# Performance work log

Hardware: AMD Instinct MI355X
Metric: run time of the kernel (lower is better)

## Reference

```python
import jax, jax.numpy as jnp
import numpy as np

N = 17
H = 8
DIRECT = np.array([[0,1],[1,2],[2,3],[0,4],[4,5],[5,6],[0,7],[7,8],[8,9],[9,10],[8,11],[11,12],[12,13],[8,14],[14,15],[15,16]])
SYM = np.array([[1,4],[2,5],[3,6],[11,14],[12,15],[13,16]])


def _base_mask(dw, sw, cw):
    # static skeleton bias: ones + direct-connect + symmetric + self-connect weights
    m = jnp.ones((N, N), jnp.float32)
    m = m.at[DIRECT[:, 0], DIRECT[:, 1]].add(dw)
    m = m.at[SYM[:, 0], SYM[:, 1]].add(sw)
    m = m.at[SYM[:, 1], SYM[:, 0]].add(sw)
    return m + cw * jnp.eye(N, dtype=jnp.float32)


def _ln_custom(x, g, b, eps=1e-6):
    # custom LayerNorm: unbiased std (torch .std default), eps added to std
    mu = x.mean(-1, keepdims=True)
    var = ((x - mu) ** 2).sum(-1, keepdims=True) / (x.shape[-1] - 1)
    return g * (x - mu) / (jnp.sqrt(var) + eps) + b


def _ln_std(x, g, b, eps=1e-5):
    # standard nn.LayerNorm (biased var, eps inside sqrt)
    mu = x.mean(-1, keepdims=True)
    var = ((x - mu) ** 2).mean(-1, keepdims=True)
    return g * (x - mu) * jax.lax.rsqrt(var + eps) + b


def _forward(mask, x, pre_3d, c, wq, bq, wk, bk, wv, bv, wo, bo, sa_w1, sa_b1, sa_g1, sa_sb1, sa_w2, sa_b2, sa_g2, sa_sb2, jrp_w, jrp_b, direct_w, sym_w, self_w, dyn_scale, A_hat, g1_w, g1_b, g2_w, g2_b, n1_g, n1_b, n2_g, n2_b, ada1_w, ada1_b, ada2_w, ada2_b):
    B, _, D = x.shape
    dk = D // H
    inv = 1.0 / np.sqrt(dk)
    mflag = (mask == 0)[:, None]                       # [B,1,N,N]
    sil_c = jax.nn.silu(c)
    for i in range(wq.shape[0]):                       # small fixed layer count
        # --- sublayer 0: adaLN-modulated skeleton-biased self-attention ---
        sh1, sc1, gt1 = jnp.split(sil_c @ ada1_w[i] + ada1_b[i], 3, axis=2)
        xin = _ln_custom(x, n1_g[i], n1_b[i]) * (1 + sc1) + sh1
        Q = (pre_3d @ wq[i] + bq[i]).reshape(B, N, H, dk).transpose(0, 2, 1, 3)
        K = (xin @ wk[i] + bk[i]).reshape(B, N, H, dk).transpose(0, 2, 1, 3)
        V = (xin @ wv[i] + bv[i]).reshape(B, N, H, dk).transpose(0, 2, 1, 3)
        scores = jnp.einsum('bhqd,bhkd->bhqk', Q, K) * inv
        # dynamic skeleton mask from query features (pre_3d)
        jf = jax.nn.relu(_ln_std(pre_3d @ sa_w1[i] + sa_b1[i], sa_g1[i], sa_sb1[i]))
        jf = jax.nn.relu(_ln_std(jf @ sa_w2[i] + sa_b2[i], sa_g2[i], sa_sb2[i]))
        dyn = jax.nn.sigmoid(jf @ jrp_w[i] + jrp_b[i]) * dyn_scale[i]   # [B,N,N]
        skel = _base_mask(direct_w[i], sym_w[i], self_w[i])[None] + dyn
        guided = jnp.where(mflag, -1e9, scores * skel[:, None])
        p = jax.nn.softmax(guided, axis=-1)
        att = jnp.einsum('bhqk,bhkd->bhqd', p, V).transpose(0, 2, 1, 3).reshape(B, N, D)
        x = x + gt1 * (att @ wo[i] + bo[i])
        # --- sublayer 1: adaLN-modulated GraphNet (2 Laplacian gconvs) ---
        sh2, sc2, gt2 = jnp.split(sil_c @ ada2_w[i] + ada2_b[i], 3, axis=2)
        y = _ln_custom(x, n2_g[i], n2_b[i]) * (1 + sc2) + sh2
        a = A_hat[i]
        dh = (a.sum(0) + 1e-5) ** -0.5                  # column-degree^{-1/2}
        Lm = dh[:, None] * a * dh[None, :]
        y0 = jax.nn.relu(jnp.einsum('ij,bjd->bid', Lm, y) @ g1_w[i] + g1_b[i])
        y1 = jnp.einsum('ij,bjd->bid', Lm, y0) @ g2_w[i] + g2_b[i]
        x = x + gt2 * y1
    return x


def setup_inputs():
    B, D, Lyr = 4096, 256, 2
    ki = iter(jax.random.split(jax.random.key(0), 32))
    rn = lambda *s: jax.random.normal(next(ki), s, jnp.float32) * 0.02
    z = lambda *s: jnp.zeros(s, jnp.float32)
    o = lambda *s: jnp.ones(s, jnp.float32)
    return {
        'x': jax.random.normal(next(ki), (B, N, D), jnp.float32),
        'pre_3d': jax.random.normal(next(ki), (B, N, D), jnp.float32),
        'c': jax.random.normal(next(ki), (B, N, D), jnp.float32),
        'mask': jnp.ones((B, N, N), jnp.int32),
        'wq': rn(Lyr, D, D), 'bq': z(Lyr, D),
        'wk': rn(Lyr, D, D), 'bk': z(Lyr, D),
        'wv': rn(Lyr, D, D), 'bv': z(Lyr, D),
        'wo': rn(Lyr, D, D), 'bo': z(Lyr, D),
        'sa_w1': rn(Lyr, D, D // 2), 'sa_b1': z(Lyr, D // 2),
        'sa_g1': o(Lyr, D // 2), 'sa_sb1': z(Lyr, D // 2),
        'sa_w2': rn(Lyr, D // 2, D // 4), 'sa_b2': z(Lyr, D // 4),
        'sa_g2': o(Lyr, D // 4), 'sa_sb2': z(Lyr, D // 4),
        'jrp_w': rn(Lyr, D // 4, N), 'jrp_b': z(Lyr, N),
        'direct_w': jnp.full((Lyr,), 2.0, jnp.float32),
        'sym_w': jnp.full((Lyr,), 1.5, jnp.float32),
        'self_w': jnp.full((Lyr,), 3.0, jnp.float32),
        'dyn_scale': jnp.full((Lyr,), 0.5, jnp.float32),
        'A_hat': jnp.tile(jnp.eye(N, dtype=jnp.float32)[None], (Lyr, 1, 1)),
        'g1_w': rn(Lyr, D, 2 * D), 'g1_b': z(Lyr, 2 * D),
        'g2_w': rn(Lyr, 2 * D, D), 'g2_b': z(Lyr, D),
        'n1_g': o(Lyr, D), 'n1_b': z(Lyr, D),
        'n2_g': o(Lyr, D), 'n2_b': z(Lyr, D),
        'ada1_w': rn(Lyr, D, 3 * D), 'ada1_b': z(Lyr, 3 * D),
        'ada2_w': rn(Lyr, D, 3 * D), 'ada2_b': z(Lyr, 3 * D),
    }


def reference(x, pre_3d, c, mask, wq, bq, wk, bk, wv, bv, wo, bo, sa_w1, sa_b1, sa_g1, sa_sb1, sa_w2, sa_b2, sa_g2, sa_sb2, jrp_w, jrp_b, direct_w, sym_w, self_w, dyn_scale, A_hat, g1_w, g1_b, g2_w, g2_b, n1_g, n1_b, n2_g, n2_b, ada1_w, ada1_b, ada2_w, ada2_b):
    return _forward(mask, x, pre_3d, c, wq, bq, wk, bk, wv, bv, wo, bo, sa_w1, sa_b1, sa_g1, sa_sb1, sa_w2, sa_b2, sa_g2, sa_sb2, jrp_w, jrp_b, direct_w, sym_w, self_w, dyn_scale, A_hat, g1_w, g1_b, g2_w, g2_b, n1_g, n1_b, n2_g, n2_b, ada1_w, ada1_b, ada2_w, ada2_b)
```

## Files before the change

kernel.cpp:

```cpp
#include <hip/hip_runtime.h>
#include <stdint.h>


#define BATCH 4096
#define NJ 17
#define NHEAD 8

typedef __bf16 bf16x8 __attribute__((ext_vector_type(8)));
typedef float f32x4 __attribute__((ext_vector_type(4)));

__device__ __forceinline__ float bf2f(unsigned short u){
  union { unsigned int i; float f; } v; v.i = ((unsigned int)u) << 16; return v.f;
}
__device__ __forceinline__ unsigned short f2bf(float f){
  union { float f; unsigned int i; } v; v.f = f;
  unsigned int i = v.i;
  return (unsigned short)((i + 0x7fffu + ((i >> 16) & 1u)) >> 16);
}
__device__ __forceinline__ float blo(unsigned int v){ union{unsigned int i;float f;}x; x.i=v<<16; return x.f; }
__device__ __forceinline__ float bhi(unsigned int v){ union{unsigned int i;float f;}x; x.i=v&0xffff0000u; return x.f; }

__device__ __forceinline__ void gload_lds16(const void* g, void* l) {
  __builtin_amdgcn_global_load_lds(
      (const __attribute__((address_space(1))) unsigned int*)g,
      (__attribute__((address_space(3))) unsigned int*)l, 16, 0, 0);
}

__global__ __launch_bounds__(256) void prep_kernel(
    const float* __restrict__ pre, const float* __restrict__ c,
    unsigned short* __restrict__ pre_bf, unsigned short* __restrict__ silc_bf)
{
  size_t i = (size_t)(blockIdx.x*256 + threadIdx.x)*4;
  float4 p = *(const float4*)(pre + i);
  float4 cv = *(const float4*)(c + i);
  float s0 = cv.x/(1.f+__expf(-cv.x));
  float s1 = cv.y/(1.f+__expf(-cv.y));
  float s2 = cv.z/(1.f+__expf(-cv.z));
  float s3 = cv.w/(1.f+__expf(-cv.w));
  uint2 po, so;
  po.x = (unsigned)f2bf(p.x) | ((unsigned)f2bf(p.y)<<16);
  po.y = (unsigned)f2bf(p.z) | ((unsigned)f2bf(p.w)<<16);
  so.x = (unsigned)f2bf(s0) | ((unsigned)f2bf(s1)<<16);
  so.y = (unsigned)f2bf(s2) | ((unsigned)f2bf(s3)<<16);
  *(uint2*)(pre_bf + i) = po;
  *(uint2*)(silc_bf + i) = so;
}

struct TJob { const float* src; unsigned short* dst; int K; int N; };
struct TJobs { TJob j[22]; };

__global__ __launch_bounds__(256) void transpose_kernel(TJobs jobs)
{
  TJob jb = jobs.j[blockIdx.y];
  int total = jb.K * jb.N;
  int idx = blockIdx.x*256 + threadIdx.x;
  if (idx >= total) return;
  int n = idx / jb.K;
  int k = idx - n*jb.K;
  jb.dst[idx] = f2bf(jb.src[(size_t)k*jb.N + n]);
}

__global__ void lm_kernel(const float* __restrict__ A_hat, float* __restrict__ LmOut)
{
  int L = blockIdx.x;
  const float* a = A_hat + L*289;
  float* Lm = LmOut + L*289;
  __shared__ float dh[17];
  int t = threadIdx.x;
  if (t < 17) {
    float s = 0;
    for (int i = 0; i < 17; i++) s += a[i*17 + t];
    dh[t] = 1.0f/sqrtf(s + 1e-5f);
  }
  __syncthreads();
  for (int i = t; i < 289; i += 64) {
    int qq = i/17, jj = i - qq*17;
    Lm[i] = dh[qq]*a[i]*dh[jj];
  }
}

__global__ __launch_bounds__(256) void lnmod_kernel(
    const float* __restrict__ x, const unsigned short* __restrict__ shsc,
    const float* __restrict__ g, const float* __restrict__ b,
    unsigned short* __restrict__ out)
{
  int row = blockIdx.x*4 + (threadIdx.x>>6);
  int lane = threadIdx.x & 63;
  const float4 v = *(const float4*)(x + (size_t)row*256 + lane*4);
  float s = v.x+v.y+v.z+v.w;
#pragma unroll
  for (int o=32;o;o>>=1) s += __shfl_down(s,o,64);
  float mu = __shfl(s,0,64) * (1.f/256.f);
  float d0=v.x-mu,d1=v.y-mu,d2=v.z-mu,d3=v.w-mu;
  float qq = d0*d0+d1*d1+d2*d2+d3*d3;
#pragma unroll
  for (int o=32;o;o>>=1) qq += __shfl_down(qq,o,64);
  qq = __shfl(qq,0,64);
  float rstd = 1.f/(sqrtf(qq*(1.f/255.f)) + 1e-6f);
  int c = lane*4;
  const float4 gv = *(const float4*)(g + c);
  const float4 bv = *(const float4*)(b + c);
  const uint2 shp = *(const uint2*)(shsc + (size_t)row*512 + c);
  const uint2 scp = *(const uint2*)(shsc + (size_t)row*512 + 256 + c);
  float o0 = (gv.x*d0*rstd + bv.x)*(1.f+blo(scp.x)) + blo(shp.x);
  float o1 = (gv.y*d1*rstd + bv.y)*(1.f+bhi(scp.x)) + bhi(shp.x);
  float o2 = (gv.z*d2*rstd + bv.z)*(1.f+blo(scp.y)) + blo(shp.y);
  float o3 = (gv.w*d3*rstd + bv.w)*(1.f+bhi(scp.y)) + bhi(shp.y);
  uint2 ov;
  ov.x = (unsigned)f2bf(o0) | ((unsigned)f2bf(o1)<<16);
  ov.y = (unsigned)f2bf(o2) | ((unsigned)f2bf(o3)<<16);
  *(uint2*)(out + (size_t)row*256 + c) = ov;
}

template<int C>
__global__ __launch_bounds__(256) void lnstd_relu_kernel(
    unsigned short* __restrict__ io, const float* __restrict__ g, const float* __restrict__ b)
{
  constexpr int EPL = C/64;
  int row = blockIdx.x*4 + (threadIdx.x>>6);
  int lane = threadIdx.x & 63;
  unsigned short* rp = io + (size_t)row*C + lane*EPL;
  float v[EPL];
  if constexpr (EPL == 2) { unsigned int u = *(const unsigned int*)rp; v[0]=blo(u); v[1]=bhi(u); }
  else { v[0] = bf2f(rp[0]); }
  float s = 0;
#pragma unroll
  for (int e=0;e<EPL;e++) s += v[e];
#pragma unroll
  for (int o=32;o;o>>=1) s += __shfl_down(s,o,64);
  float mu = __shfl(s,0,64) * (1.f/C);
  float qq = 0;
#pragma unroll
  for (int e=0;e<EPL;e++){ float d=v[e]-mu; qq += d*d; }
#pragma unroll
  for (int o=32;o;o>>=1) qq += __shfl_down(qq,o,64);
  qq = __shfl(qq,0,64);
  float rstd = rsqrtf(qq*(1.f/C) + 1e-5f);
  unsigned short ov[EPL];
#pragma unroll
  for (int e=0;e<EPL;e++){
    int ccol = lane*EPL + e;
    float o = fmaxf(g[ccol]*(v[e]-mu)*rstd + b[ccol], 0.f);
    ov[e] = f2bf(o);
  }
  if constexpr (EPL==2){ *(unsigned int*)rp = (unsigned)ov[0] | ((unsigned)ov[1]<<16); }
  else rp[0] = ov[0];
}

__global__ __launch_bounds__(256) void skel_kernel(
    const unsigned short* __restrict__ jf2, const unsigned short* __restrict__ jrpt,
    const float* __restrict__ jrp_b,
    const float* __restrict__ dwp, const float* __restrict__ swp,
    const float* __restrict__ cwp, const float* __restrict__ dsp,
    float* __restrict__ skel)
{
  int gid = blockIdx.x*256 + threadIdx.x;
  int row = gid / 17;
  int k = gid - row*17;
  int q = row % 17;
  const uint4* a = (const uint4*)(jf2 + (size_t)row*64);
  const uint4* w = (const uint4*)(jrpt + k*64);
  float acc = jrp_b[k];
#pragma unroll
  for (int c = 0; c < 8; c++) {
    uint4 ua = a[c], uw = w[c];
    acc += blo(ua.x)*blo(uw.x) + bhi(ua.x)*bhi(uw.x)
         + blo(ua.y)*blo(uw.y) + bhi(ua.y)*bhi(uw.y)
         + blo(ua.z)*blo(uw.z) + bhi(ua.z)*bhi(uw.z)
         + blo(ua.w)*blo(uw.w) + bhi(ua.w)*bhi(uw.w);
  }
  float sig = 1.f/(1.f + __expf(-acc));
  float base = 1.f;
  const int dqa[16] = {0,1,2,0,4,5,0,7,8,9,8,11,12,8,14,15};
  const int dka[16] = {1,2,3,4,5,6,7,8,9,10,11,12,13,14,15,16};
#pragma unroll
  for (int t = 0; t < 16; t++) if (q==dqa[t] && k==dka[t]) base += dwp[0];
  const int s0a[6] = {1,2,3,11,12,13};
  const int s1a[6] = {4,5,6,14,15,16};
#pragma unroll
  for (int t = 0; t < 6; t++) if ((q==s0a[t]&&k==s1a[t])||(q==s1a[t]&&k==s0a[t])) base += swp[0];
  if (q==k) base += cwp[0];
  skel[gid] = base + sig*dsp[0];
}

__device__ __forceinline__ void load32(const unsigned short* p, float* f){
  const uint4* p4 = (const uint4*)p;
#pragma unroll
  for (int c=0;c<4;c++){
    uint4 u=p4[c];
    f[c*8+0]=blo(u.x); f[c*8+1]=bhi(u.x); f[c*8+2]=blo(u.y); f[c*8+3]=bhi(u.y);
    f[c*8+4]=blo(u.z); f[c*8+5]=bhi(u.z); f[c*8+6]=blo(u.w); f[c*8+7]=bhi(u.w);
  }
}

__global__ __launch_bounds__(256) void attn_kernel(
    const unsigned short* Q, const unsigned short* __restrict__ Kb,
    const unsigned short* __restrict__ V, const float* __restrict__ skel,
    const int* __restrict__ mask, unsigned short* att)
{
  int tid = blockIdx.x*256 + threadIdx.x;
  int b = tid / 136;
  int r = tid - b*136;
  int h = r / 17;
  int q = r - h*17;
  size_t rq = ((size_t)(b*17+q))*256 + h*32;
  float qv[32];
  load32(Q + rq, qv);
  const float* sk = skel + (size_t)(b*17+q)*17;
  const int* mk = mask + (size_t)b*289 + q*17;
  float p[17];
  float mx = -3e38f;
#pragma unroll
  for (int k = 0; k < 17; k++) {
    const uint4* kp = (const uint4*)(Kb + ((size_t)(b*17+k))*256 + h*32);
    float s = 0;
#pragma unroll
    for (int c = 0; c < 4; c++) {
      uint4 u = kp[c];
      s += qv[c*8+0]*blo(u.x) + qv[c*8+1]*bhi(u.x)
         + qv[c*8+2]*blo(u.y) + qv[c*8+3]*bhi(u.y)
         + qv[c*8+4]*blo(u.z) + qv[c*8+5]*bhi(u.z)
         + qv[c*8+6]*blo(u.w) + qv[c*8+7]*bhi(u.w);
    }
    s *= 0.17677669529663687f;
    float gvl = (mk[k]==0) ? -1e9f : s*sk[k];
    p[k] = gvl;
    mx = fmaxf(mx, gvl);
  }
  float sum = 0;
#pragma unroll
  for (int k = 0; k < 17; k++){ p[k] = __expf(p[k]-mx); sum += p[k]; }
  float inv = 1.f/sum;
  float acc[32];
#pragma unroll
  for (int d=0; d<32; d++) acc[d]=0;
#pragma unroll
  for (int k = 0; k < 17; k++) {
    float pk = p[k]*inv;
    const uint4* vp = (const uint4*)(V + ((size_t)(b*17+k))*256 + h*32);
#pragma unroll
    for (int c=0;c<4;c++){
      uint4 u=vp[c];
      acc[c*8+0] += pk*blo(u.x); acc[c*8+1] += pk*bhi(u.x);
      acc[c*8+2] += pk*blo(u.y); acc[c*8+3] += pk*bhi(u.y);
      acc[c*8+4] += pk*blo(u.z); acc[c*8+5] += pk*bhi(u.z);
      acc[c*8+6] += pk*blo(u.w); acc[c*8+7] += pk*bhi(u.w);
    }
  }
  uint4 o[4];
#pragma unroll
  for (int c=0;c<4;c++){
    o[c].x = (unsigned)f2bf(acc[c*8+0]) | ((unsigned)f2bf(acc[c*8+1])<<16);
    o[c].y = (unsigned)f2bf(acc[c*8+2]) | ((unsigned)f2bf(acc[c*8+3])<<16);
    o[c].z = (unsigned)f2bf(acc[c*8+4]) | ((unsigned)f2bf(acc[c*8+5])<<16);
    o[c].w = (unsigned)f2bf(acc[c*8+6]) | ((unsigned)f2bf(acc[c*8+7])<<16);
  }
  uint4* op = (uint4*)(att + rq);
#pragma unroll
  for (int c=0;c<4;c++) op[c] = o[c];
}

template<int D>
__global__ __launch_bounds__(256) void lmapply_kernel(
    unsigned short* __restrict__ io, const float* __restrict__ Lm)
{
  __shared__ unsigned short ys[17*D];
  __shared__ float lms[289];
  int b = blockIdx.x;
  int tid = threadIdx.x;
  unsigned short* base = io + (size_t)b*17*D;
  constexpr int CH = 17*D/8;
  for (int i = tid; i < CH; i += 256) ((uint4*)ys)[i] = ((const uint4*)base)[i];
  for (int i = tid; i < 289; i += 256) lms[i] = Lm[i];
  __syncthreads();
#pragma unroll
  for (int c0 = 0; c0 < D; c0 += 256) {
    int c = c0 + tid;
    float yv[17];
#pragma unroll
    for (int j = 0; j < 17; j++) yv[j] = bf2f(ys[j*D + c]);
#pragma unroll
    for (int qi = 0; qi < 17; qi++) {
      float a = 0;
#pragma unroll
      for (int j = 0; j < 17; j++) a += lms[qi*17+j]*yv[j];
      base[qi*D + c] = f2bf(a);
    }
  }
}

template<int TM, int TN, int EPI>
__global__ __launch_bounds__(256) void gemm_kernel(
    const unsigned short* __restrict__ A, const unsigned short* __restrict__ Bt,
    const float* __restrict__ bias, unsigned short* __restrict__ outbf,
    float* __restrict__ x_io, const unsigned short* __restrict__ gt,
    int N, int K)
{
  int lane = threadIdx.x & 63;
  int wave = threadIdx.x >> 6;
  int lm = lane & 15, quad = lane >> 4;
  int wm0 = blockIdx.x*(2*TM*16) + (wave>>1)*(TM*16);
  int wn0 = blockIdx.y*(2*TN*16) + (wave&1)*(TN*16);
  const unsigned short* pa[TM];
  const unsigned short* pb[TN];
#pragma unroll
  for (int t=0;t<TM;t++) pa[t] = A + (size_t)(wm0 + t*16 + lm)*K + quad*8;
#pragma unroll
  for (int t=0;t<TN;t++) pb[t] = Bt + (size_t)(wn0 + t*16 + lm)*K + quad*8;
  f32x4 acc[TM][TN] = {};
  for (int kc = 0; kc < K; kc += 32) {
    bf16x8 af[TM], bfv[TN];
#pragma unroll
    for (int t=0;t<TM;t++) af[t] = *(const bf16x8*)(pa[t] + kc);
#pragma unroll
    for (int t=0;t<TN;t++) bfv[t] = *(const bf16x8*)(pb[t] + kc);
#pragma unroll
    for (int i=0;i<TM;i++)
#pragma unroll
      for (int j=0;j<TN;j++)
        acc[i][j] = __builtin_amdgcn_mfma_f32_16x16x32_bf16(af[i], bfv[j], acc[i][j], 0, 0, 0);
  }
#pragma unroll
  for (int j=0;j<TN;j++) {
    int col = wn0 + j*16 + lm;
    float bv = bias[col];
#pragma unroll
    for (int i=0;i<TM;i++) {
      int r0 = wm0 + i*16 + quad*4;
#pragma unroll
      for (int e=0;e<4;e++) {
        int rr = r0 + e;
        float v = acc[i][j][e] + bv;
        if (EPI == 0) {
          outbf[(size_t)rr*N + col] = f2bf(v);
        } else if (EPI == 1) {
          outbf[(size_t)rr*N + col] = f2bf(fmaxf(v, 0.f));
        } else {
          size_t xi = (size_t)rr*N + col;
          x_io[xi] += bf2f(gt[(size_t)rr*256 + col]) * v;
        }
      }
    }
  }
}

template<int EPI>
__global__ __launch_bounds__(256) void gemm_lds_kernel(
    const unsigned short* __restrict__ A, const unsigned short* __restrict__ Bt,
    const float* __restrict__ bias, unsigned short* __restrict__ outbf,
    float* __restrict__ x_io, const unsigned short* __restrict__ gt,
    int N, int K)
{
  __shared__ unsigned short As[128*32];
  __shared__ unsigned short Bs[128*32];
  const int tid = threadIdx.x;
  const int lane = tid & 63;
  const int wave = tid >> 6;
  const int lm = lane & 15, quad = lane >> 4;
  const int m0 = blockIdx.y * 128;
  const int n0 = blockIdx.x * 128;
  const int wm = (wave >> 1) * 64;
  const int wn = (wave & 1) * 64;

  const int srow = tid >> 2;
  const int sslot = tid & 3;

  f32x4 acc[4][4] = {};

  for (int kc = 0; kc < K; kc += 32) {
    __syncthreads();
#pragma unroll
    for (int l = 0; l < 2; l++) {
      int r = l*64 + srow;
      int gs = sslot ^ (r & 3);
      gload_lds16(A + (size_t)(m0 + r)*K + kc + gs*8, As + (size_t)l*2048 + tid*8);
      gload_lds16(Bt + (size_t)(n0 + r)*K + kc + gs*8, Bs + (size_t)l*2048 + tid*8);
    }
    __syncthreads();

    bf16x8 af[4], bfv[4];
#pragma unroll
    for (int t = 0; t < 4; t++) {
      int ra = wm + t*16 + lm;
      af[t]  = *(const bf16x8*)(As + ra*32 + ((quad ^ (ra & 3)) << 3));
      int rb = wn + t*16 + lm;
      bfv[t] = *(const bf16x8*)(Bs + rb*32 + ((quad ^ (rb & 3)) << 3));
    }
#pragma unroll
    for (int i = 0; i < 4; i++)
#pragma unroll
      for (int j = 0; j < 4; j++)
        acc[i][j] = __builtin_amdgcn_mfma_f32_16x16x32_bf16(af[i], bfv[j], acc[i][j], 0, 0, 0);
  }

#pragma unroll
  for (int j = 0; j < 4; j++) {
    int col = n0 + wn + j*16 + lm;
    float bv = bias[col];
#pragma unroll
    for (int i = 0; i < 4; i++) {
      int r0 = m0 + wm + i*16 + quad*4;
#pragma unroll
      for (int e = 0; e < 4; e++) {
        int rr = r0 + e;
        float v = acc[i][j][e] + bv;
        if (EPI == 0) {
          outbf[(size_t)rr*N + col] = f2bf(v);
        } else if (EPI == 1) {
          outbf[(size_t)rr*N + col] = f2bf(fmaxf(v, 0.f));
        } else {
          size_t xi = (size_t)rr*N + col;
          x_io[xi] += bf2f(gt[(size_t)rr*256 + col]) * v;
        }
      }
    }
  }
}

extern "C" void kernel_launch(void* const* d_in, const int* in_sizes, int n_in,
                              void* d_out, int out_size, void* d_ws, size_t ws_size,
                              hipStream_t stream)
{
  const float* x_in = (const float*)d_in[0];
  const float* pre  = (const float*)d_in[1];
  const float* cc   = (const float*)d_in[2];
  const int*   mask = (const int*)d_in[3];
  const float* wq = (const float*)d_in[4];   const float* bq = (const float*)d_in[5];
  const float* wk = (const float*)d_in[6];   const float* bk = (const float*)d_in[7];
  const float* wv = (const float*)d_in[8];   const float* bv = (const float*)d_in[9];
  const float* wo = (const float*)d_in[10];  const float* bo = (const float*)d_in[11];
  const float* sa_w1 = (const float*)d_in[12]; const float* sa_b1 = (const float*)d_in[13];
  const float* sa_g1 = (const float*)d_in[14]; const float* sa_sb1 = (const float*)d_in[15];
  const float* sa_w2 = (const float*)d_in[16]; const float* sa_b2 = (const float*)d_in[17];
  const float* sa_g2 = (const float*)d_in[18]; const float* sa_sb2 = (const float*)d_in[19];
  const float* jrp_w = (const float*)d_in[20]; const float* jrp_b = (const float*)d_in[21];
  const float* dwp = (const float*)d_in[22]; const float* swp = (const float*)d_in[23];
  const float* cwp = (const float*)d_in[24]; const float* dsp = (const float*)d_in[25];
  const float* A_hat = (const float*)d_in[26];
  const float* g1w = (const float*)d_in[27]; const float* g1b = (const float*)d_in[28];
  const float* g2w = (const float*)d_in[29]; const float* g2b = (const float*)d_in[30];
  const float* n1g = (const float*)d_in[31]; const float* n1b = (const float*)d_in[32];
  const float* n2g = (const float*)d_in[33]; const float* n2b = (const float*)d_in[34];
  const float* ada1w = (const float*)d_in[35]; const float* ada1b = (const float*)d_in[36];
  const float* ada2w = (const float*)d_in[37]; const float* ada2b = (const float*)d_in[38];

  char* ws = (char*)d_ws;
  size_t off = 0;
  auto alloc = [&](size_t bytes)->char* {
    char* p = ws + off; off = (off + bytes + 255) & ~(size_t)255; return p;
  };

  TJobs jobs;
  int ji = 0;
  auto addjob = [&](const float* src, int Kd, int Nd)->unsigned short* {
    unsigned short* dst = (unsigned short*)alloc((size_t)Kd*Nd*2);
    jobs.j[ji].src = src; jobs.j[ji].dst = dst; jobs.j[ji].K = Kd; jobs.j[ji].N = Nd;
    ji++;
    return dst;
  };
  unsigned short *t_ada1[2], *t_wq[2], *t_wk[2], *t_wv[2], *t_wo[2],
                 *t_sa1[2], *t_sa2[2], *t_jrp[2], *t_g1[2], *t_g2[2], *t_ada2[2];
  for (int L = 0; L < 2; L++) {
    t_ada1[L] = addjob(ada1w + (size_t)L*256*768, 256, 768);
    t_wq[L]   = addjob(wq + (size_t)L*65536, 256, 256);
    t_wk[L]   = addjob(wk + (size_t)L*65536, 256, 256);
    t_wv[L]   = addjob(wv + (size_t)L*65536, 256, 256);
    t_wo[L]   = addjob(wo + (size_t)L*65536, 256, 256);
    t_sa1[L]  = addjob(sa_w1 + (size_t)L*256*128, 256, 128);
    t_sa2[L]  = addjob(sa_w2 + (size_t)L*128*64, 128, 64);
    t_jrp[L]  = addjob(jrp_w + (size_t)L*64*17, 64, 17);
    t_g1[L]   = addjob(g1w + (size_t)L*256*512, 256, 512);
    t_g2[L]   = addjob(g2w + (size_t)L*512*256, 512, 256);
    t_ada2[L] = addjob(ada2w + (size_t)L*256*768, 256, 768);
  }
  float* lmbuf = (float*)alloc(2*289*4);
  size_t fixed_bytes = off;

  int chunkB = BATCH;
  for (; chunkB > 256; chunkB >>= 1) {
    size_t R = (size_t)chunkB * NJ;
    if (fixed_bytes + R*3652 + 8*256 <= ws_size) break;
  }
  const size_t R = (size_t)chunkB * NJ;
  const int nchunks = BATCH / chunkB;

  unsigned short* pre_bf  = (unsigned short*)alloc(R*256*2);
  unsigned short* silc_bf = (unsigned short*)alloc(R*256*2);
  unsigned short* xinb    = (unsigned short*)alloc(R*256*2);
  unsigned short* qbuf    = (unsigned short*)alloc(R*256*2);
  unsigned short* gtbuf   = (unsigned short*)alloc(R*256*2);
  unsigned short* kvb     = (unsigned short*)alloc(R*512*2);
  float*          skelb   = (float*)alloc(R*NJ*4);

  unsigned short* jf1 = xinb;
  unsigned short* jf2 = xinb + R*128;
  unsigned short* Kbuf = kvb;
  unsigned short* Vbuf = kvb + R*256;

  float* xout = (float*)d_out;
  hipMemcpyAsync(xout, x_in, (size_t)BATCH*NJ*256*4, hipMemcpyDeviceToDevice, stream);
  transpose_kernel<<<dim3(768, 22), 256, 0, stream>>>(jobs);
  lm_kernel<<<2, 64, 0, stream>>>(A_hat, lmbuf);

  const int gX = (int)(R/128);
  const int g4 = (int)(R/4);

  for (int ch = 0; ch < nchunks; ch++) {
    const size_t r0 = (size_t)ch * R;
    const float* pre_c = pre + r0*256;
    const float* cc_c  = cc + r0*256;
    const int* mask_c  = mask + (size_t)ch*chunkB*289;
    float* x_c = xout + r0*256;

    prep_kernel<<<g4, 256, 0, stream>>>(pre_c, cc_c, pre_bf, silc_bf);

    for (int L = 0; L < 2; L++) {
      gemm_lds_kernel<0><<<dim3(4,gX),256,0,stream>>>(silc_bf, t_ada1[L], ada1b + L*768, kvb, nullptr, nullptr, 512, 256);
      gemm_lds_kernel<0><<<dim3(2,gX),256,0,stream>>>(silc_bf, t_ada1[L] + 512*256, ada1b + L*768 + 512, gtbuf, nullptr, nullptr, 256, 256);
      lnmod_kernel<<<g4,256,0,stream>>>(x_c, kvb, n1g + L*256, n1b + L*256, xinb);
      gemm_lds_kernel<0><<<dim3(2,gX),256,0,stream>>>(pre_bf, t_wq[L], bq + L*256, qbuf, nullptr, nullptr, 256, 256);
      gemm_lds_kernel<0><<<dim3(2,gX),256,0,stream>>>(xinb, t_wk[L], bk + L*256, Kbuf, nullptr, nullptr, 256, 256);
      gemm_lds_kernel<0><<<dim3(2,gX),256,0,stream>>>(xinb, t_wv[L], bv + L*256, Vbuf, nullptr, nullptr, 256, 256);
      gemm_lds_kernel<0><<<dim3(1,gX),256,0,stream>>>(pre_bf, t_sa1[L], sa_b1 + L*128, jf1, nullptr, nullptr, 128, 256);
      lnstd_relu_kernel<128><<<g4,256,0,stream>>>(jf1, sa_g1 + L*128, sa_sb1 + L*128);
      gemm_kernel<4,2,0><<<dim3(gX,1),256,0,stream>>>(jf1, t_sa2[L], sa_b2 + L*64, jf2, nullptr, nullptr, 64, 128);
      lnstd_relu_kernel<64><<<g4,256,0,stream>>>(jf2, sa_g2 + L*64, sa_sb2 + L*64);
      skel_kernel<<<(int)(R*NJ/256),256,0,stream>>>(jf2, t_jrp[L], jrp_b + L*17, dwp+L, swp+L, cwp+L, dsp+L, skelb);
      attn_kernel<<<chunkB*136/256,256,0,stream>>>(qbuf, Kbuf, Vbuf, skelb, mask_c, qbuf);
      gemm_lds_kernel<3><<<dim3(2,gX),256,0,stream>>>(qbuf, t_wo[L], bo + L*256, nullptr, x_c, gtbuf, 256, 256);
      gemm_lds_kernel<0><<<dim3(4,gX),256,0,stream>>>(silc_bf, t_ada2[L], ada2b + L*768, kvb, nullptr, nullptr, 512, 256);
      gemm_lds_kernel<0><<<dim3(2,gX),256,0,stream>>>(silc_bf, t_ada2[L] + 512*256, ada2b + L*768 + 512, gtbuf, nullptr, nullptr, 256, 256);
      lnmod_kernel<<<g4,256,0,stream>>>(x_c, kvb, n2g + L*256, n2b + L*256, xinb);
      lmapply_kernel<256><<<chunkB,256,0,stream>>>(xinb, lmbuf + L*289);
      gemm_lds_kernel<1><<<dim3(4,gX),256,0,stream>>>(xinb, t_g1[L], g1b + L*512, kvb, nullptr, nullptr, 512, 256);
      lmapply_kernel<512><<<chunkB,256,0,stream>>>(kvb, lmbuf + L*289);
      gemm_lds_kernel<3><<<dim3(2,gX),256,0,stream>>>(kvb, t_g2[L], g2b + L*256, nullptr, x_c, gtbuf, 256, 512);
    }
  }
}
```

Measured before the change: 1.776 ms.

## Triple-buffer GEMM LDS loads, merge sibling GEMMs, remap blocks across XCDs

```diff
diff --git a/kernel.cpp b/kernel.cpp
--- a/kernel.cpp
+++ b/kernel.cpp
@@ -194,8 +194,8 @@
 }
 
 __global__ __launch_bounds__(256) void attn_kernel(
-    const unsigned short* Q, const unsigned short* __restrict__ Kb,
-    const unsigned short* __restrict__ V, const float* __restrict__ skel,
+    const unsigned short* Q, const unsigned short* __restrict__ KV,
+    const float* __restrict__ skel,
     const int* __restrict__ mask, unsigned short* att)
 {
   int tid = blockIdx.x*256 + threadIdx.x;
@@ -212,7 +212,7 @@
   float mx = -3e38f;
 #pragma unroll
   for (int k = 0; k < 17; k++) {
-    const uint4* kp = (const uint4*)(Kb + ((size_t)(b*17+k))*256 + h*32);
+    const uint4* kp = (const uint4*)(KV + ((size_t)(b*17+k))*512 + h*32);
     float s = 0;
 #pragma unroll
     for (int c = 0; c < 4; c++) {
@@ -237,7 +237,7 @@
 #pragma unroll
   for (int k = 0; k < 17; k++) {
     float pk = p[k]*inv;
-    const uint4* vp = (const uint4*)(V + ((size_t)(b*17+k))*256 + h*32);
+    const uint4* vp = (const uint4*)(KV + ((size_t)(b*17+k))*512 + 256 + h*32);
 #pragma unroll
     for (int c=0;c<4;c++){
       uint4 u=vp[c];
@@ -347,56 +347,82 @@
 template<int EPI>
 __global__ __launch_bounds__(256) void gemm_lds_kernel(
     const unsigned short* __restrict__ A, const unsigned short* __restrict__ Bt,
-    const float* __restrict__ bias, unsigned short* __restrict__ outbf,
+    const float* __restrict__ bias, const float* __restrict__ bias2,
+    unsigned short* __restrict__ out1, int ld1,
+    unsigned short* __restrict__ out2, int ld2, int splitN,
     float* __restrict__ x_io, const unsigned short* __restrict__ gt,
-    int N, int K)
-{
-  __shared__ unsigned short As[128*32];
-  __shared__ unsigned short Bs[128*32];
+    int K)
+{
+  __shared__ unsigned short As[3][128*32];
+  __shared__ unsigned short Bs[3][128*32];
   const int tid = threadIdx.x;
   const int lane = tid & 63;
   const int wave = tid >> 6;
   const int lm = lane & 15, quad = lane >> 4;
-  const int m0 = blockIdx.y * 128;
-  const int n0 = blockIdx.x * 128;
+
+  const int gx = gridDim.x;
+  const int nwg = gx * (int)gridDim.y;
+  int flat = (int)blockIdx.y * gx + (int)blockIdx.x;
+  int xcd = flat & 7, idx = flat >> 3;
+  int qd = nwg >> 3, rm = nwg & 7;
+  int wg = (xcd < rm ? xcd*(qd+1) : rm*(qd+1) + (xcd-rm)*qd) + idx;
+  int by = wg / gx, bx = wg - by*gx;
+  const int m0 = by * 128;
+  const int n0 = bx * 128;
   const int wm = (wave >> 1) * 64;
   const int wn = (wave & 1) * 64;
 
   const int srow = tid >> 2;
   const int sslot = tid & 3;
 
+  auto stage = [&](int buf, int kc) {
+#pragma unroll
+    for (int l = 0; l < 2; l++) {
+      int rr = l*64 + srow;
+      int gs = sslot ^ (rr & 3);
+      gload_lds16(A + (size_t)(m0 + rr)*K + kc + gs*8, &As[buf][l*2048 + tid*8]);
+      gload_lds16(Bt + (size_t)(n0 + rr)*K + kc + gs*8, &Bs[buf][l*2048 + tid*8]);
+    }
+  };
+
+  const int nt = K >> 5;
+  stage(0, 0);
+  stage(1, 32);
+
   f32x4 acc[4][4] = {};
-
-  for (int kc = 0; kc < K; kc += 32) {
-    __syncthreads();
-#pragma unroll
-    for (int l = 0; l < 2; l++) {
-      int r = l*64 + srow;
-      int gs = sslot ^ (r & 3);
-      gload_lds16(A + (size_t)(m0 + r)*K + kc + gs*8, As + (size_t)l*2048 + tid*8);
-      gload_lds16(Bt + (size_t)(n0 + r)*K + kc + gs*8, Bs + (size_t)l*2048 + tid*8);
-    }
-    __syncthreads();
-
+  for (int t = 0; t < nt; t++) {
+    if (t + 2 < nt) {
+      stage((t+2)%3, (t+2)*32);
+      asm volatile("s_waitcnt vmcnt(8)" ::: "memory");
+    } else if (t + 1 < nt) {
+      asm volatile("s_waitcnt vmcnt(4)" ::: "memory");
+    } else {
+      asm volatile("s_waitcnt vmcnt(0)" ::: "memory");
+    }
+    __builtin_amdgcn_s_barrier();
+
+    const unsigned short* as_ = As[t % 3];
+    const unsigned short* bs_ = Bs[t % 3];
     bf16x8 af[4], bfv[4];
 #pragma unroll
-    for (int t = 0; t < 4; t++) {
-      int ra = wm + t*16 + lm;
-      af[t]  = *(const bf16x8*)(As + ra*32 + ((quad ^ (ra & 3)) << 3));
-      int rb = wn + t*16 + lm;
-      bfv[t] = *(const bf16x8*)(Bs + rb*32 + ((quad ^ (rb & 3)) << 3));
+    for (int tt = 0; tt < 4; tt++) {
+      int ra = wm + tt*16 + lm;
+      af[tt]  = *(const bf16x8*)(as_ + ra*32 + ((quad ^ (ra & 3)) << 3));
+      int rb = wn + tt*16 + lm;
+      bfv[tt] = *(const bf16x8*)(bs_ + rb*32 + ((quad ^ (rb & 3)) << 3));
     }
 #pragma unroll
     for (int i = 0; i < 4; i++)
 #pragma unroll
       for (int j = 0; j < 4; j++)
         acc[i][j] = __builtin_amdgcn_mfma_f32_16x16x32_bf16(af[i], bfv[j], acc[i][j], 0, 0, 0);
+    __builtin_amdgcn_s_barrier();
   }
 
 #pragma unroll
   for (int j = 0; j < 4; j++) {
     int col = n0 + wn + j*16 + lm;
-    float bv = bias[col];
+    float bv = (bias2 && col >= splitN) ? bias2[col - splitN] : bias[col];
 #pragma unroll
     for (int i = 0; i < 4; i++) {
       int r0 = m0 + wm + i*16 + quad*4;
@@ -405,12 +431,13 @@
         int rr = r0 + e;
         float v = acc[i][j][e] + bv;
         if (EPI == 0) {
-          outbf[(size_t)rr*N + col] = f2bf(v);
+          if (out2 && col >= splitN) out2[(size_t)rr*ld2 + (col - splitN)] = f2bf(v);
+          else                       out1[(size_t)rr*ld1 + col] = f2bf(v);
         } else if (EPI == 1) {
-          outbf[(size_t)rr*N + col] = f2bf(fmaxf(v, 0.f));
+          out1[(size_t)rr*ld1 + col] = f2bf(fmaxf(v, 0.f));
         } else {
-          size_t xi = (size_t)rr*N + col;
-          x_io[xi] += bf2f(gt[(size_t)rr*256 + col]) * v;
+          size_t xi = (size_t)rr*256 + col;
+          x_io[xi] += bf2f(gt[xi]) * v;
         }
       }
     }
@@ -427,7 +454,7 @@
   const int*   mask = (const int*)d_in[3];
   const float* wq = (const float*)d_in[4];   const float* bq = (const float*)d_in[5];
   const float* wk = (const float*)d_in[6];   const float* bk = (const float*)d_in[7];
-  const float* wv = (const float*)d_in[8];   const float* bv = (const float*)d_in[9];
+  const float* wv = (const float*)d_in[8];   const float* bvz = (const float*)d_in[9];
   const float* wo = (const float*)d_in[10];  const float* bo = (const float*)d_in[11];
   const float* sa_w1 = (const float*)d_in[12]; const float* sa_b1 = (const float*)d_in[13];
   const float* sa_g1 = (const float*)d_in[14]; const float* sa_sb1 = (const float*)d_in[15];
@@ -452,26 +479,33 @@
 
   TJobs jobs;
   int ji = 0;
-  auto addjob = [&](const float* src, int Kd, int Nd)->unsigned short* {
-    unsigned short* dst = (unsigned short*)alloc((size_t)Kd*Nd*2);
+  auto addjob = [&](const float* src, unsigned short* dst, int Kd, int Nd) {
     jobs.j[ji].src = src; jobs.j[ji].dst = dst; jobs.j[ji].K = Kd; jobs.j[ji].N = Nd;
     ji++;
-    return dst;
   };
-  unsigned short *t_ada1[2], *t_wq[2], *t_wk[2], *t_wv[2], *t_wo[2],
-                 *t_sa1[2], *t_sa2[2], *t_jrp[2], *t_g1[2], *t_g2[2], *t_ada2[2];
+  unsigned short *t_ada1[2], *t_qsa[2], *t_kv[2], *t_wo[2],
+                 *t_sa2[2], *t_jrp[2], *t_g1[2], *t_g2[2], *t_ada2[2];
   for (int L = 0; L < 2; L++) {
-    t_ada1[L] = addjob(ada1w + (size_t)L*256*768, 256, 768);
-    t_wq[L]   = addjob(wq + (size_t)L*65536, 256, 256);
-    t_wk[L]   = addjob(wk + (size_t)L*65536, 256, 256);
-    t_wv[L]   = addjob(wv + (size_t)L*65536, 256, 256);
-    t_wo[L]   = addjob(wo + (size_t)L*65536, 256, 256);
-    t_sa1[L]  = addjob(sa_w1 + (size_t)L*256*128, 256, 128);
-    t_sa2[L]  = addjob(sa_w2 + (size_t)L*128*64, 128, 64);
-    t_jrp[L]  = addjob(jrp_w + (size_t)L*64*17, 64, 17);
-    t_g1[L]   = addjob(g1w + (size_t)L*256*512, 256, 512);
-    t_g2[L]   = addjob(g2w + (size_t)L*512*256, 512, 256);
-    t_ada2[L] = addjob(ada2w + (size_t)L*256*768, 256, 768);
+    t_ada1[L] = (unsigned short*)alloc((size_t)768*256*2);
+    addjob(ada1w + (size_t)L*256*768, t_ada1[L], 256, 768);
+    t_qsa[L] = (unsigned short*)alloc((size_t)384*256*2);
+    addjob(wq + (size_t)L*65536, t_qsa[L], 256, 256);
+    addjob(sa_w1 + (size_t)L*256*128, t_qsa[L] + 256*256, 256, 128);
+    t_kv[L] = (unsigned short*)alloc((size_t)512*256*2);
+    addjob(wk + (size_t)L*65536, t_kv[L], 256, 256);
+    addjob(wv + (size_t)L*65536, t_kv[L] + 256*256, 256, 256);
+    t_wo[L] = (unsigned short*)alloc((size_t)256*256*2);
+    addjob(wo + (size_t)L*65536, t_wo[L], 256, 256);
+    t_sa2[L] = (unsigned short*)alloc((size_t)64*128*2);
+    addjob(sa_w2 + (size_t)L*128*64, t_sa2[L], 128, 64);
+    t_jrp[L] = (unsigned short*)alloc((size_t)17*64*2);
+    addjob(jrp_w + (size_t)L*64*17, t_jrp[L], 64, 17);
+    t_g1[L] = (unsigned short*)alloc((size_t)512*256*2);
+    addjob(g1w + (size_t)L*256*512, t_g1[L], 256, 512);
+    t_g2[L] = (unsigned short*)alloc((size_t)256*512*2);
+    addjob(g2w + (size_t)L*512*256, t_g2[L], 512, 256);
+    t_ada2[L] = (unsigned short*)alloc((size_t)768*256*2);
+    addjob(ada2w + (size_t)L*256*768, t_ada2[L], 256, 768);
   }
   float* lmbuf = (float*)alloc(2*289*4);
   size_t fixed_bytes = off;
@@ -494,8 +528,6 @@
 
   unsigned short* jf1 = xinb;
   unsigned short* jf2 = xinb + R*128;
-  unsigned short* Kbuf = kvb;
-  unsigned short* Vbuf = kvb + R*256;
 
   float* xout = (float*)d_out;
   hipMemcpyAsync(xout, x_in, (size_t)BATCH*NJ*256*4, hipMemcpyDeviceToDevice, stream);
@@ -515,26 +547,29 @@
     prep_kernel<<<g4, 256, 0, stream>>>(pre_c, cc_c, pre_bf, silc_bf);
 
     for (int L = 0; L < 2; L++) {
-      gemm_lds_kernel<0><<<dim3(4,gX),256,0,stream>>>(silc_bf, t_ada1[L], ada1b + L*768, kvb, nullptr, nullptr, 512, 256);
-      gemm_lds_kernel<0><<<dim3(2,gX),256,0,stream>>>(silc_bf, t_ada1[L] + 512*256, ada1b + L*768 + 512, gtbuf, nullptr, nullptr, 256, 256);
+      gemm_lds_kernel<0><<<dim3(6,gX),256,0,stream>>>(silc_bf, t_ada1[L],
+          ada1b + L*768, nullptr, kvb, 512, gtbuf, 256, 512, nullptr, nullptr, 256);
       lnmod_kernel<<<g4,256,0,stream>>>(x_c, kvb, n1g + L*256, n1b + L*256, xinb);
-      gemm_lds_kernel<0><<<dim3(2,gX),256,0,stream>>>(pre_bf, t_wq[L], bq + L*256, qbuf, nullptr, nullptr, 256, 256);
-      gemm_lds_kernel<0><<<dim3(2,gX),256,0,stream>>>(xinb, t_wk[L], bk + L*256, Kbuf, nullptr, nullptr, 256, 256);
-      gemm_lds_kernel<0><<<dim3(2,gX),256,0,stream>>>(xinb, t_wv[L], bv + L*256, Vbuf, nullptr, nullptr, 256, 256);
-      gemm_lds_kernel<0><<<dim3(1,gX),256,0,stream>>>(pre_bf, t_sa1[L], sa_b1 + L*128, jf1, nullptr, nullptr, 128, 256);
+      gemm_lds_kernel<0><<<dim3(4,gX),256,0,stream>>>(xinb, t_kv[L],
+          bk + L*256, bvz + L*256, kvb, 512, nullptr, 0, 256, nullptr, nullptr, 256);
+      gemm_lds_kernel<0><<<dim3(3,gX),256,0,stream>>>(pre_bf, t_qsa[L],
+          bq + L*256, sa_b1 + L*128, qbuf, 256, jf1, 128, 256, nullptr, nullptr, 256);
       lnstd_relu_kernel<128><<<g4,256,0,stream>>>(jf1, sa_g1 + L*128, sa_sb1 + L*128);
       gemm_kernel<4,2,0><<<dim3(gX,1),256,0,stream>>>(jf1, t_sa2[L], sa_b2 + L*64, jf2, nullptr, nullptr, 64, 128);
       lnstd_relu_kernel<64><<<g4,256,0,stream>>>(jf2, sa_g2 + L*64, sa_sb2 + L*64);
       skel_kernel<<<(int)(R*NJ/256),256,0,stream>>>(jf2, t_jrp[L], jrp_b + L*17, dwp+L, swp+L, cwp+L, dsp+L, skelb);
-      attn_kernel<<<chunkB*136/256,256,0,stream>>>(qbuf, Kbuf, Vbuf, skelb, mask_c, qbuf);
-      gemm_lds_kernel<3><<<dim3(2,gX),256,0,stream>>>(qbuf, t_wo[L], bo + L*256, nullptr, x_c, gtbuf, 256, 256);
-      gemm_lds_kernel<0><<<dim3(4,gX),256,0,stream>>>(silc_bf, t_ada2[L], ada2b + L*768, kvb, nullptr, nullptr, 512, 256);
-      gemm_lds_kernel<0><<<dim3(2,gX),256,0,stream>>>(silc_bf, t_ada2[L] + 512*256, ada2b + L*768 + 512, gtbuf, nullptr, nullptr, 256, 256);
+      attn_kernel<<<chunkB*136/256,256,0,stream>>>(qbuf, kvb, skelb, mask_c, qbuf);
+      gemm_lds_kernel<3><<<dim3(2,gX),256,0,stream>>>(qbuf, t_wo[L],
+          bo + L*256, nullptr, nullptr, 0, nullptr, 0, 0, x_c, gtbuf, 256);
+      gemm_lds_kernel<0><<<dim3(6,gX),256,0,stream>>>(silc_bf, t_ada2[L],
+          ada2b + L*768, nullptr, kvb, 512, gtbuf, 256, 512, nullptr, nullptr, 256);
       lnmod_kernel<<<g4,256,0,stream>>>(x_c, kvb, n2g + L*256, n2b + L*256, xinb);
       lmapply_kernel<256><<<chunkB,256,0,stream>>>(xinb, lmbuf + L*289);
-      gemm_lds_kernel<1><<<dim3(4,gX),256,0,stream>>>(xinb, t_g1[L], g1b + L*512, kvb, nullptr, nullptr, 512, 256);
+      gemm_lds_kernel<1><<<dim3(4,gX),256,0,stream>>>(xinb, t_g1[L],
+          g1b + L*512, nullptr, kvb, 512, nullptr, 0, 0, nullptr, nullptr, 256);
       lmapply_kernel<512><<<chunkB,256,0,stream>>>(kvb, lmbuf + L*289);
-      gemm_lds_kernel<3><<<dim3(2,gX),256,0,stream>>>(kvb, t_g2[L], g2b + L*256, nullptr, x_c, gtbuf, 256, 512);
-    }
-  }
-}
+      gemm_lds_kernel<3><<<dim3(2,gX),256,0,stream>>>(kvb, t_g2[L],
+          g2b + L*256, nullptr, nullptr, 0, nullptr, 0, 0, x_c, gtbuf, 512);
+    }
+  }
+}
```

New measurement: 1.649 ms. 7.2% less time.
